# Optimization experiments

Hardware: AMD Instinct MI355X
Metric: run time of the kernel (lower is better)

Reference implementation:

```python
import jax, jax.numpy as jnp
import numpy as np

T, B, D, Hd = 512, 64, 1024, 1024
SIGMA = 0.01


def setup_inputs() -> dict:
    key = jax.random.key(0)
    ks = jax.random.split(key, 9)
    inp = {
        "inputs": jax.random.normal(ks[0], (T, B, D), dtype=jnp.float32),
        "H0": jnp.zeros((B, Hd), dtype=jnp.float32),
        "C0": jnp.zeros((B, Hd), dtype=jnp.float32),
    }
    names_x = ["W_xi", "W_xf", "W_xo", "W_xc"]
    names_h = ["W_hi", "W_hf", "W_ho", "W_hc"]
    for i, n in enumerate(names_x):
        inp[n] = jax.random.normal(ks[1 + i], (D, Hd), dtype=jnp.float32) * SIGMA
    for i, n in enumerate(names_h):
        inp[n] = jax.random.normal(ks[5 + i], (Hd, Hd), dtype=jnp.float32) * SIGMA
    for n in ["b_i", "b_f", "b_o", "b_c"]:
        inp[n] = jnp.zeros((Hd,), dtype=jnp.float32)
    return inp


def reference(inputs, H0, C0, W_xi, W_xf, W_xo, W_xc,
              W_hi, W_hf, W_ho, W_hc, b_i, b_f, b_o, b_c):
    # Fuse the 4 input-projection and 4 hidden-projection GEMMs into 2 GEMMs
    # per step (same math as 8 separate matmuls, just concatenated).
    Wx = jnp.concatenate([W_xi, W_xf, W_xo, W_xc], axis=1)   # [D, 4H]
    Wh = jnp.concatenate([W_hi, W_hf, W_ho, W_hc], axis=1)   # [H, 4H]
    b = jnp.concatenate([b_i, b_f, b_o, b_c], axis=0)        # [4H]
    nh = b_i.shape[0]

    def step(carry, X):
        H, C = carry
        gates = X @ Wx + H @ Wh + b                          # [B, 4H]
        i, f, o, g = jnp.split(gates, 4, axis=1)
        I = jax.nn.sigmoid(i)
        F = jax.nn.sigmoid(f)
        O = jax.nn.sigmoid(o)
        C_tilde = jnp.tanh(g)
        C_new = F * C + I * C_tilde
        H_new = O * jnp.tanh(C_new)
        return (H_new, C_new), H_new

    (H_f, C_f), outputs = jax.lax.scan(step, (H0, C0), inputs)  # outputs [T, B, H]
    return outputs, (H_f, C_f)
```

## Files before the change

### kernel.cpp

```cpp
#include <hip/hip_runtime.h>
#include <cstdint>

#define TT 512
#define BB 64
#define DD 1024
#define HH 1024
#define NWG 128

typedef __attribute__((ext_vector_type(8))) __bf16 bf16x8;
typedef __attribute__((ext_vector_type(4))) float f32x4;

#define WS_XQ    0
#define WS_WHB   67108864ULL
#define WS_HQ    83886080ULL
#define WS_FLAGS 151126016ULL
#define FLAGS_BYTES (256 * 128)

__device__ __forceinline__ unsigned short f2bf(float f) {
    unsigned int u = __float_as_uint(f);
    u = (u + 0x7fffu + ((u >> 16) & 1u)) >> 16;
    return (unsigned short)u;
}

__device__ __forceinline__ float sigm(float x) {
    return 1.0f / (1.0f + __expf(-x));
}
__device__ __forceinline__ float tanh_f(float x) {
    float a = fabsf(x);
    float e = __expf(-2.0f * a);
    float t = (1.0f - e) / (1.0f + e);
    return copysignf(t, x);
}

__device__ __forceinline__ unsigned long long pack4bf(float a, float b, float c, float d) {
    return (unsigned long long)f2bf(a)
         | ((unsigned long long)f2bf(b) << 16)
         | ((unsigned long long)f2bf(c) << 32)
         | ((unsigned long long)f2bf(d) << 48);
}

__global__ void cvt_x(const float* __restrict__ X, unsigned short* __restrict__ Xq) {
    int i = blockIdx.x * blockDim.x + threadIdx.x;
    const int n8 = TT * BB * DD / 8;
    if (i >= n8) return;
    const float4* s = (const float4*)X;
    float4 a = s[2 * i], b = s[2 * i + 1];
    union { unsigned short u[8]; uint4 q; } r;
    r.u[0] = f2bf(a.x); r.u[1] = f2bf(a.y); r.u[2] = f2bf(a.z); r.u[3] = f2bf(a.w);
    r.u[4] = f2bf(b.x); r.u[5] = f2bf(b.y); r.u[6] = f2bf(b.z); r.u[7] = f2bf(b.w);
    ((uint4*)Xq)[i] = r.q;
}

__global__ void pack_w(const float* __restrict__ Wxi, const float* __restrict__ Wxf,
                       const float* __restrict__ Wxo, const float* __restrict__ Wxc,
                       const float* __restrict__ Whi, const float* __restrict__ Whf,
                       const float* __restrict__ Who, const float* __restrict__ Whc,
                       unsigned short* __restrict__ WhB) {
    int tid = blockIdx.x * blockDim.x + threadIdx.x;
    int lane = tid & 63;
    int ct   = (tid >> 6) & 1;
    int s    = (tid >> 7) & 15;
    int kq   = (tid >> 11) & 3;
    int wg   = tid >> 13;
    int col  = ct * 16 + (lane & 15);
    int gate = col >> 3;
    int h    = wg * 8 + (col & 7);
    int kb   = kq * 512 + s * 32 + ((lane >> 4) & 3) * 8;

    const float* Wx[4] = {Wxi, Wxf, Wxo, Wxc};
    const float* Wh[4] = {Whi, Whf, Who, Whc};
    const float* W = (kb < 1024) ? (Wx[gate] + (size_t)kb * HH + h)
                                 : (Wh[gate] + (size_t)(kb - 1024) * HH + h);
    union { unsigned short u[8]; uint4 q; } r;
#pragma unroll
    for (int m = 0; m < 8; ++m) r.u[m] = f2bf(W[(size_t)m * HH]);
    *(uint4*)(WhB + (size_t)tid * 8) = r.q;
}

__global__ void __launch_bounds__(512, 2)
lstm_seq(const unsigned short* __restrict__ Xq, const unsigned short* __restrict__ WhB,
         unsigned short* __restrict__ Hq, int* flags,
         const float* __restrict__ H0, const float* __restrict__ C0,
         const float* __restrict__ bi, const float* __restrict__ bfp,
         const float* __restrict__ bo, const float* __restrict__ bc,
         float* __restrict__ out) {
    __shared__ float gpart[4][64][36];

    const int wg    = blockIdx.x;
    const int tid   = threadIdx.x;
    const int wv    = tid >> 6;
    const int lane  = tid & 63;
    const int quad  = lane >> 4;
    const int l15   = lane & 15;
    const int rhalf = wv & 1;
    const bool isH  = (wv >= 4);
    const int kq    = isH ? 2 + ((wv - 4) >> 1) : (wv >> 1);
    const int arow0 = rhalf * 32 + l15;

    const bool isAct = (wv == 4) || (wv == 5);
    const int aidx   = tid - 256;
    const int r2     = aidx >> 1;
    const int ahalf  = aidx & 1;
    const int hcol0  = wg * 8 + ahalf * 4;

    float Bi[4], Bf[4], Bo[4], Bc[4], Cr[4];
    if (isAct) {
#pragma unroll
        for (int j = 0; j < 4; ++j) {
            Bi[j] = bi[hcol0 + j];
            Bf[j] = bfp[hcol0 + j];
            Bo[j] = bo[hcol0 + j];
            Bc[j] = bc[hcol0 + j];
            Cr[j] = C0[(size_t)r2 * HH + hcol0 + j];
        }
    }

    bf16x8 Breg[16][2];
    {
        const unsigned short* wp = WhB + (size_t)(wg * 4 + kq) * (16 * 2 * 64 * 8);
#pragma unroll
        for (int s = 0; s < 16; ++s)
#pragma unroll
            for (int ct = 0; ct < 2; ++ct)
                Breg[s][ct] = *(const bf16x8*)(wp + ((s * 2 + ct) * 64 + lane) * 8);
    }

    if (tid < 64) {
        const float* s = H0 + (size_t)tid * HH + wg * 8;
        unsigned long long a = pack4bf(s[0], s[1], s[2], s[3]);
        unsigned long long b = pack4bf(s[4], s[5], s[6], s[7]);
        unsigned long long* d = (unsigned long long*)(Hq + (size_t)tid * HH + wg * 8);
        __hip_atomic_store(d,     a, __ATOMIC_RELAXED, __HIP_MEMORY_SCOPE_AGENT);
        __hip_atomic_store(d + 1, b, __ATOMIC_RELAXED, __HIP_MEMORY_SCOPE_AGENT);
    }
    if (wv == 0) {
        asm volatile("s_waitcnt vmcnt(0)" ::: "memory");
        if (lane < 2)
            __hip_atomic_store(flags + ((wg * 2 + lane) * 8 + 0) * 4, 1,
                               __ATOMIC_RELAXED, __HIP_MEMORY_SCOPE_AGENT);
    }

    for (int t = 0; t < TT; ++t) {
        f32x4 a00 = {0.f,0.f,0.f,0.f}, a01 = {0.f,0.f,0.f,0.f};
        f32x4 a10 = {0.f,0.f,0.f,0.f}, a11 = {0.f,0.f,0.f,0.f};

        if (!isH) {
            const unsigned short* xb = Xq + ((size_t)(t * BB + arow0)) * DD + kq * 512 + quad * 8;
#pragma unroll
            for (int s = 0; s < 16; ++s) {
                bf16x8 af0 = *(const bf16x8*)(xb + s * 32);
                bf16x8 af1 = *(const bf16x8*)(xb + 16 * DD + s * 32);
                a00 = __builtin_amdgcn_mfma_f32_16x16x32_bf16(af0, Breg[s][0], a00, 0, 0, 0);
                a01 = __builtin_amdgcn_mfma_f32_16x16x32_bf16(af0, Breg[s][1], a01, 0, 0, 0);
                a10 = __builtin_amdgcn_mfma_f32_16x16x32_bf16(af1, Breg[s][0], a10, 0, 0, 0);
                a11 = __builtin_amdgcn_mfma_f32_16x16x32_bf16(af1, Breg[s][1], a11, 0, 0, 0);
            }
        } else {
            const int kqh  = kq - 2;
            const int slot = t & 7;
            const int thr  = t + 1;
            const int* fp  = flags + (((kqh * 64 + lane) * 2 + rhalf) * 8 + slot) * 4;
            const unsigned short* hb = Hq + ((size_t)(t * BB + arow0)) * HH + kqh * 512 + quad * 8;

            int myf = __hip_atomic_load(fp, __ATOMIC_RELAXED, __HIP_MEMORY_SCOPE_AGENT);
            unsigned long long got = __ballot(myf >= thr);
            while ((got & 0xFFFFFFFFull) != 0xFFFFFFFFull) {
                __builtin_amdgcn_s_sleep(2);
                if (myf < thr)
                    myf = __hip_atomic_load(fp, __ATOMIC_RELAXED, __HIP_MEMORY_SCOPE_AGENT);
                got = __ballot(myf >= thr);
            }
            asm volatile("" ::: "memory");
            {
                bf16x8 af[8][2];
#pragma unroll
                for (int s = 0; s < 8; ++s) {
                    af[s][0] = *(const bf16x8*)(hb + s * 32);
                    af[s][1] = *(const bf16x8*)(hb + 16 * HH + s * 32);
                }
#pragma unroll
                for (int s = 0; s < 8; ++s) {
                    a00 = __builtin_amdgcn_mfma_f32_16x16x32_bf16(af[s][0], Breg[s][0], a00, 0, 0, 0);
                    a01 = __builtin_amdgcn_mfma_f32_16x16x32_bf16(af[s][0], Breg[s][1], a01, 0, 0, 0);
                    a10 = __builtin_amdgcn_mfma_f32_16x16x32_bf16(af[s][1], Breg[s][0], a10, 0, 0, 0);
                    a11 = __builtin_amdgcn_mfma_f32_16x16x32_bf16(af[s][1], Breg[s][1], a11, 0, 0, 0);
                }
            }

            while (got != ~0ull) {
                __builtin_amdgcn_s_sleep(2);
                if (myf < thr)
                    myf = __hip_atomic_load(fp, __ATOMIC_RELAXED, __HIP_MEMORY_SCOPE_AGENT);
                got = __ballot(myf >= thr);
            }
            asm volatile("" ::: "memory");
            {
                bf16x8 af[8][2];
#pragma unroll
                for (int s = 0; s < 8; ++s) {
                    af[s][0] = *(const bf16x8*)(hb + (8 + s) * 32);
                    af[s][1] = *(const bf16x8*)(hb + 16 * HH + (8 + s) * 32);
                }
#pragma unroll
                for (int s = 0; s < 8; ++s) {
                    a00 = __builtin_amdgcn_mfma_f32_16x16x32_bf16(af[s][0], Breg[8 + s][0], a00, 0, 0, 0);
                    a01 = __builtin_amdgcn_mfma_f32_16x16x32_bf16(af[s][0], Breg[8 + s][1], a01, 0, 0, 0);
                    a10 = __builtin_amdgcn_mfma_f32_16x16x32_bf16(af[s][1], Breg[8 + s][0], a10, 0, 0, 0);
                    a11 = __builtin_amdgcn_mfma_f32_16x16x32_bf16(af[s][1], Breg[8 + s][1], a11, 0, 0, 0);
                }
            }
        }

#pragma unroll
        for (int r = 0; r < 4; ++r) {
            int row0 = rhalf * 32 + quad * 4 + r;
            gpart[kq][row0][l15]           = a00[r];
            gpart[kq][row0][16 + l15]      = a01[r];
            gpart[kq][row0 + 16][l15]      = a10[r];
            gpart[kq][row0 + 16][16 + l15] = a11[r];
        }
        __syncthreads();

        if (isAct) {
            float hv[4];
#pragma unroll
            for (int j = 0; j < 4; ++j) {
                const int c = ahalf * 4 + j;
                float gi = gpart[0][r2][c]      + gpart[1][r2][c]
                         + gpart[2][r2][c]      + gpart[3][r2][c]      + Bi[j];
                float gf = gpart[0][r2][8 + c]  + gpart[1][r2][8 + c]
                         + gpart[2][r2][8 + c]  + gpart[3][r2][8 + c]  + Bf[j];
                float go = gpart[0][r2][16 + c] + gpart[1][r2][16 + c]
                         + gpart[2][r2][16 + c] + gpart[3][r2][16 + c] + Bo[j];
                float gc = gpart[0][r2][24 + c] + gpart[1][r2][24 + c]
                         + gpart[2][r2][24 + c] + gpart[3][r2][24 + c] + Bc[j];
                float I = sigm(gi), F = sigm(gf), O = sigm(go), G = tanh_f(gc);
                Cr[j] = F * Cr[j] + I * G;
                hv[j] = O * tanh_f(Cr[j]);
            }
            unsigned long long pk = pack4bf(hv[0], hv[1], hv[2], hv[3]);
            __hip_atomic_store(
                (unsigned long long*)(Hq + ((size_t)(t + 1) * BB + r2) * HH + hcol0),
                pk, __ATOMIC_RELAXED, __HIP_MEMORY_SCOPE_AGENT);
            asm volatile("s_waitcnt vmcnt(0)" ::: "memory");
            if (lane == 0)
                __hip_atomic_store(
                    flags + ((wg * 2 + (wv - 4)) * 8 + ((t + 1) & 7)) * 4, t + 2,
                    __ATOMIC_RELAXED, __HIP_MEMORY_SCOPE_AGENT);
            float4 v = make_float4(hv[0], hv[1], hv[2], hv[3]);
            *(float4*)(out + ((size_t)t * BB + r2) * HH + hcol0) = v;
            if (t == TT - 1) {
                *(float4*)(out + (size_t)TT * BB * HH + (size_t)r2 * HH + hcol0) = v;
            }
        }
        __syncthreads();
    }

    if (isAct) {
        float* cf = out + (size_t)TT * BB * HH + (size_t)BB * HH;
        *(float4*)(cf + (size_t)r2 * HH + hcol0) = make_float4(Cr[0], Cr[1], Cr[2], Cr[3]);
    }
}

extern "C" void kernel_launch(void* const* d_in, const int* in_sizes, int n_in,
                              void* d_out, int out_size, void* d_ws, size_t ws_size,
                              hipStream_t stream) {
    const float* X   = (const float*)d_in[0];
    const float* H0  = (const float*)d_in[1];
    const float* C0  = (const float*)d_in[2];
    const float* Wxi = (const float*)d_in[3];
    const float* Wxf = (const float*)d_in[4];
    const float* Wxo = (const float*)d_in[5];
    const float* Wxc = (const float*)d_in[6];
    const float* Whi = (const float*)d_in[7];
    const float* Whf = (const float*)d_in[8];
    const float* Who = (const float*)d_in[9];
    const float* Whc = (const float*)d_in[10];
    const float* bi  = (const float*)d_in[11];
    const float* bf_ = (const float*)d_in[12];
    const float* bo  = (const float*)d_in[13];
    const float* bc  = (const float*)d_in[14];

    char* ws = (char*)d_ws;
    unsigned short* Xq  = (unsigned short*)(ws + WS_XQ);
    unsigned short* WhB = (unsigned short*)(ws + WS_WHB);
    unsigned short* Hq  = (unsigned short*)(ws + WS_HQ);
    int* flags          = (int*)(ws + WS_FLAGS);

    hipMemsetAsync(flags, 0, FLAGS_BYTES, stream);

    hipLaunchKernelGGL(cvt_x, dim3(TT * BB * DD / 8 / 256), dim3(256), 0, stream, X, Xq);
    hipLaunchKernelGGL(pack_w, dim3(4096), dim3(256), 0, stream,
                       Wxi, Wxf, Wxo, Wxc, Whi, Whf, Who, Whc, WhB);
    hipLaunchKernelGGL(lstm_seq, dim3(NWG), dim3(512), 0, stream,
                       Xq, WhB, Hq, flags, H0, C0, bi, bf_, bo, bc, (float*)d_out);
}
```

Measured before the change: 5.024 ms.

## Use producer-tiled H buffer, per-slice flag waits, and double-buffered gate partials

Stores each workgroup's bf16 hidden-state slice as a contiguous 512-byte tile per row-half, in MFMA A-fragment order, instead of row-major. The recurrent MFMA loop now waits only on the four producer flags each k-slice needs, so it can start computing as soon as the earliest producers finish. The second per-step __syncthreads is removed by double-buffering the LDS gate-partial array. The aim is to shorten the per-timestep critical path of cross-workgroup synchronisation. The cost is more fine-grained polling and a 2x larger LDS buffer.

```diff
diff --git a/kernel.cpp b/kernel.cpp
--- a/kernel.cpp
+++ b/kernel.cpp
@@ -12,8 +12,9 @@
 
 #define WS_XQ    0
 #define WS_WHB   67108864ULL
-#define WS_HQ    83886080ULL
+#define WS_HQ2   83886080ULL
 #define WS_FLAGS 151126016ULL
+#define HQ2_BYTES ((size_t)(TT + 1) * NWG * 2 * 512)
 #define FLAGS_BYTES (256 * 128)
 
 __device__ __forceinline__ unsigned short f2bf(float f) {
@@ -79,12 +80,12 @@
 
 __global__ void __launch_bounds__(512, 2)
 lstm_seq(const unsigned short* __restrict__ Xq, const unsigned short* __restrict__ WhB,
-         unsigned short* __restrict__ Hq, int* flags,
+         unsigned char* __restrict__ Hq2, int* flags,
          const float* __restrict__ H0, const float* __restrict__ C0,
          const float* __restrict__ bi, const float* __restrict__ bfp,
          const float* __restrict__ bo, const float* __restrict__ bc,
          float* __restrict__ out) {
-    __shared__ float gpart[4][64][36];
+    __shared__ float gpart[2][4][64][36];
 
     const int wg    = blockIdx.x;
     const int tid   = threadIdx.x;
@@ -125,15 +126,16 @@
                 Breg[s][ct] = *(const bf16x8*)(wp + ((s * 2 + ct) * 64 + lane) * 8);
     }
 
-    if (tid < 64) {
-        const float* s = H0 + (size_t)tid * HH + wg * 8;
-        unsigned long long a = pack4bf(s[0], s[1], s[2], s[3]);
-        unsigned long long b = pack4bf(s[4], s[5], s[6], s[7]);
-        unsigned long long* d = (unsigned long long*)(Hq + (size_t)tid * HH + wg * 8);
-        __hip_atomic_store(d,     a, __ATOMIC_RELAXED, __HIP_MEMORY_SCOPE_AGENT);
-        __hip_atomic_store(d + 1, b, __ATOMIC_RELAXED, __HIP_MEMORY_SCOPE_AGENT);
-    }
     if (wv == 0) {
+#pragma unroll
+        for (int a = 0; a < 2; ++a) {
+            int row = a * 32 + (lane >> 1);
+            const float* s = H0 + (size_t)row * HH + wg * 8 + (lane & 1) * 4;
+            unsigned long long v = pack4bf(s[0], s[1], s[2], s[3]);
+            unsigned long long* d =
+                (unsigned long long*)(Hq2 + (((size_t)wg) * 2 + a) * 512) + lane;
+            __hip_atomic_store(d, v, __ATOMIC_RELAXED, __HIP_MEMORY_SCOPE_AGENT);
+        }
         asm volatile("s_waitcnt vmcnt(0)" ::: "memory");
         if (lane < 2)
             __hip_atomic_store(flags + ((wg * 2 + lane) * 8 + 0) * 4, 1,
@@ -141,6 +143,7 @@
     }
 
     for (int t = 0; t < TT; ++t) {
+        const int pb = t & 1;
         f32x4 a00 = {0.f,0.f,0.f,0.f}, a01 = {0.f,0.f,0.f,0.f};
         f32x4 a10 = {0.f,0.f,0.f,0.f}, a11 = {0.f,0.f,0.f,0.f};
 
@@ -160,64 +163,38 @@
             const int slot = t & 7;
             const int thr  = t + 1;
             const int* fp  = flags + (((kqh * 64 + lane) * 2 + rhalf) * 8 + slot) * 4;
-            const unsigned short* hb = Hq + ((size_t)(t * BB + arow0)) * HH + kqh * 512 + quad * 8;
+            const unsigned char* tb =
+                Hq2 + (((size_t)t * NWG + kqh * 64) * 2 + rhalf) * 512;
 
             int myf = __hip_atomic_load(fp, __ATOMIC_RELAXED, __HIP_MEMORY_SCOPE_AGENT);
             unsigned long long got = __ballot(myf >= thr);
-            while ((got & 0xFFFFFFFFull) != 0xFFFFFFFFull) {
-                __builtin_amdgcn_s_sleep(2);
-                if (myf < thr)
-                    myf = __hip_atomic_load(fp, __ATOMIC_RELAXED, __HIP_MEMORY_SCOPE_AGENT);
-                got = __ballot(myf >= thr);
-            }
-            asm volatile("" ::: "memory");
-            {
-                bf16x8 af[8][2];
-#pragma unroll
-                for (int s = 0; s < 8; ++s) {
-                    af[s][0] = *(const bf16x8*)(hb + s * 32);
-                    af[s][1] = *(const bf16x8*)(hb + 16 * HH + s * 32);
+#pragma unroll
+            for (int s = 0; s < 16; ++s) {
+                const unsigned long long need = 0xFull << (s * 4);
+                while ((got & need) != need) {
+                    __builtin_amdgcn_s_sleep(1);
+                    if (myf < thr)
+                        myf = __hip_atomic_load(fp, __ATOMIC_RELAXED, __HIP_MEMORY_SCOPE_AGENT);
+                    got = __ballot(myf >= thr);
                 }
-#pragma unroll
-                for (int s = 0; s < 8; ++s) {
-                    a00 = __builtin_amdgcn_mfma_f32_16x16x32_bf16(af[s][0], Breg[s][0], a00, 0, 0, 0);
-                    a01 = __builtin_amdgcn_mfma_f32_16x16x32_bf16(af[s][0], Breg[s][1], a01, 0, 0, 0);
-                    a10 = __builtin_amdgcn_mfma_f32_16x16x32_bf16(af[s][1], Breg[s][0], a10, 0, 0, 0);
-                    a11 = __builtin_amdgcn_mfma_f32_16x16x32_bf16(af[s][1], Breg[s][1], a11, 0, 0, 0);
-                }
-            }
-
-            while (got != ~0ull) {
-                __builtin_amdgcn_s_sleep(2);
-                if (myf < thr)
-                    myf = __hip_atomic_load(fp, __ATOMIC_RELAXED, __HIP_MEMORY_SCOPE_AGENT);
-                got = __ballot(myf >= thr);
-            }
-            asm volatile("" ::: "memory");
-            {
-                bf16x8 af[8][2];
-#pragma unroll
-                for (int s = 0; s < 8; ++s) {
-                    af[s][0] = *(const bf16x8*)(hb + (8 + s) * 32);
-                    af[s][1] = *(const bf16x8*)(hb + 16 * HH + (8 + s) * 32);
-                }
-#pragma unroll
-                for (int s = 0; s < 8; ++s) {
-                    a00 = __builtin_amdgcn_mfma_f32_16x16x32_bf16(af[s][0], Breg[8 + s][0], a00, 0, 0, 0);
-                    a01 = __builtin_amdgcn_mfma_f32_16x16x32_bf16(af[s][0], Breg[8 + s][1], a01, 0, 0, 0);
-                    a10 = __builtin_amdgcn_mfma_f32_16x16x32_bf16(af[s][1], Breg[8 + s][0], a10, 0, 0, 0);
-                    a11 = __builtin_amdgcn_mfma_f32_16x16x32_bf16(af[s][1], Breg[8 + s][1], a11, 0, 0, 0);
-                }
+                asm volatile("" ::: "memory");
+                const unsigned char* bb = tb + (size_t)(s * 4 + quad) * 1024;
+                bf16x8 af0 = *(const bf16x8*)(bb + l15 * 16);
+                bf16x8 af1 = *(const bf16x8*)(bb + (l15 + 16) * 16);
+                a00 = __builtin_amdgcn_mfma_f32_16x16x32_bf16(af0, Breg[s][0], a00, 0, 0, 0);
+                a01 = __builtin_amdgcn_mfma_f32_16x16x32_bf16(af0, Breg[s][1], a01, 0, 0, 0);
+                a10 = __builtin_amdgcn_mfma_f32_16x16x32_bf16(af1, Breg[s][0], a10, 0, 0, 0);
+                a11 = __builtin_amdgcn_mfma_f32_16x16x32_bf16(af1, Breg[s][1], a11, 0, 0, 0);
             }
         }
 
 #pragma unroll
         for (int r = 0; r < 4; ++r) {
             int row0 = rhalf * 32 + quad * 4 + r;
-            gpart[kq][row0][l15]           = a00[r];
-            gpart[kq][row0][16 + l15]      = a01[r];
-            gpart[kq][row0 + 16][l15]      = a10[r];
-            gpart[kq][row0 + 16][16 + l15] = a11[r];
+            gpart[pb][kq][row0][l15]           = a00[r];
+            gpart[pb][kq][row0][16 + l15]      = a01[r];
+            gpart[pb][kq][row0 + 16][l15]      = a10[r];
+            gpart[pb][kq][row0 + 16][16 + l15] = a11[r];
         }
         __syncthreads();
 
@@ -226,26 +203,28 @@
 #pragma unroll
             for (int j = 0; j < 4; ++j) {
                 const int c = ahalf * 4 + j;
-                float gi = gpart[0][r2][c]      + gpart[1][r2][c]
-                         + gpart[2][r2][c]      + gpart[3][r2][c]      + Bi[j];
-                float gf = gpart[0][r2][8 + c]  + gpart[1][r2][8 + c]
-                         + gpart[2][r2][8 + c]  + gpart[3][r2][8 + c]  + Bf[j];
-                float go = gpart[0][r2][16 + c] + gpart[1][r2][16 + c]
-                         + gpart[2][r2][16 + c] + gpart[3][r2][16 + c] + Bo[j];
-                float gc = gpart[0][r2][24 + c] + gpart[1][r2][24 + c]
-                         + gpart[2][r2][24 + c] + gpart[3][r2][24 + c] + Bc[j];
+                float gi = gpart[pb][0][r2][c]      + gpart[pb][1][r2][c]
+                         + gpart[pb][2][r2][c]      + gpart[pb][3][r2][c]      + Bi[j];
+                float gf = gpart[pb][0][r2][8 + c]  + gpart[pb][1][r2][8 + c]
+                         + gpart[pb][2][r2][8 + c]  + gpart[pb][3][r2][8 + c]  + Bf[j];
+                float go = gpart[pb][0][r2][16 + c] + gpart[pb][1][r2][16 + c]
+                         + gpart[pb][2][r2][16 + c] + gpart[pb][3][r2][16 + c] + Bo[j];
+                float gc = gpart[pb][0][r2][24 + c] + gpart[pb][1][r2][24 + c]
+                         + gpart[pb][2][r2][24 + c] + gpart[pb][3][r2][24 + c] + Bc[j];
                 float I = sigm(gi), F = sigm(gf), O = sigm(go), G = tanh_f(gc);
                 Cr[j] = F * Cr[j] + I * G;
                 hv[j] = O * tanh_f(Cr[j]);
             }
+            const int a = wv - 4;
+            const int w = aidx & 63;
             unsigned long long pk = pack4bf(hv[0], hv[1], hv[2], hv[3]);
-            __hip_atomic_store(
-                (unsigned long long*)(Hq + ((size_t)(t + 1) * BB + r2) * HH + hcol0),
-                pk, __ATOMIC_RELAXED, __HIP_MEMORY_SCOPE_AGENT);
+            unsigned long long* d = (unsigned long long*)
+                (Hq2 + (((size_t)(t + 1) * NWG + wg) * 2 + a) * 512) + w;
+            __hip_atomic_store(d, pk, __ATOMIC_RELAXED, __HIP_MEMORY_SCOPE_AGENT);
             asm volatile("s_waitcnt vmcnt(0)" ::: "memory");
             if (lane == 0)
                 __hip_atomic_store(
-                    flags + ((wg * 2 + (wv - 4)) * 8 + ((t + 1) & 7)) * 4, t + 2,
+                    flags + ((wg * 2 + a) * 8 + ((t + 1) & 7)) * 4, t + 2,
                     __ATOMIC_RELAXED, __HIP_MEMORY_SCOPE_AGENT);
             float4 v = make_float4(hv[0], hv[1], hv[2], hv[3]);
             *(float4*)(out + ((size_t)t * BB + r2) * HH + hcol0) = v;
@@ -253,7 +232,6 @@
                 *(float4*)(out + (size_t)TT * BB * HH + (size_t)r2 * HH + hcol0) = v;
             }
         }
-        __syncthreads();
     }
 
     if (isAct) {
@@ -284,7 +262,7 @@
     char* ws = (char*)d_ws;
     unsigned short* Xq  = (unsigned short*)(ws + WS_XQ);
     unsigned short* WhB = (unsigned short*)(ws + WS_WHB);
-    unsigned short* Hq  = (unsigned short*)(ws + WS_HQ);
+    unsigned char*  Hq2 = (unsigned char*)(ws + WS_HQ2);
     int* flags          = (int*)(ws + WS_FLAGS);
 
     hipMemsetAsync(flags, 0, FLAGS_BYTES, stream);
@@ -293,5 +271,5 @@
     hipLaunchKernelGGL(pack_w, dim3(4096), dim3(256), 0, stream,
                        Wxi, Wxf, Wxo, Wxc, Whi, Whf, Who, Whc, WhB);
     hipLaunchKernelGGL(lstm_seq, dim3(NWG), dim3(512), 0, stream,
-                       Xq, WhB, Hq, flags, H0, C0, bi, bf_, bo, bc, (float*)d_out);
-}
+                       Xq, WhB, Hq2, flags, H0, C0, bi, bf_, bo, bc, (float*)d_out);
+}
```

New measurement: 4.539 ms. 1.11x faster.
